# Performance work log

Measured on AMD Instinct MI355X. Metric: run time of the kernel, lower is better.

Reference implementation:

```python
import jax, jax.numpy as jnp
import numpy as np

B, N, D_IN, D_OUT = 8, 2048, 1024, 1024

def setup_inputs() -> dict:
    key = jax.random.key(0)
    kx, kq, kk, kv = jax.random.split(key, 4)
    scale = 1.0 / np.sqrt(D_IN)
    return {
        "x": jax.random.normal(kx, (B, N, D_IN), dtype=jnp.float32),
        "Wq": jax.random.normal(kq, (D_IN, D_OUT), dtype=jnp.float32) * scale,
        "Wk": jax.random.normal(kk, (D_IN, D_OUT), dtype=jnp.float32) * scale,
        "Wv": jax.random.normal(kv, (D_IN, D_OUT), dtype=jnp.float32) * scale,
    }

def reference(x, Wq, Wk, Wv):
    # Projections (qkv_bias=False)
    q = x @ Wq  # [B, N, d_out]
    k = x @ Wk
    v = x @ Wv
    n = x.shape[1]
    scores = jnp.einsum('bqd,bkd->bqk', q, k)  # [B, N, N]
    causal_mask = jnp.triu(jnp.ones((n, n), dtype=bool), k=1)
    scores = jnp.where(causal_mask, -jnp.inf, scores)
    inv_sqrt_d = jnp.asarray(1.0 / np.sqrt(q.shape[-1]), dtype=scores.dtype)
    attn = jax.nn.softmax(scores * inv_sqrt_d, axis=-1)
    # dropout p=0.0 -> identity
    return jnp.einsum('bqk,bkd->bqd', attn, v)
```

## Files before the change

kernel.cpp:

```cpp
#include <hip/hip_runtime.h>
#include <hip/hip_bf16.h>

#define DI __device__ __forceinline__

typedef __bf16 bf16x8 __attribute__((ext_vector_type(8)));
typedef float  f32x4  __attribute__((ext_vector_type(4)));

DI unsigned short f2bf(float f) {
    unsigned int u = __float_as_uint(f);
    u += 0x7fffu + ((u >> 16) & 1u);
    return (unsigned short)(u >> 16);
}

DI void gload16(const unsigned short* g, unsigned short* l) {
    __builtin_amdgcn_global_load_lds(
        (const __attribute__((address_space(1))) unsigned int*)g,
        (__attribute__((address_space(3))) unsigned int*)l, 16, 0, 0);
}

__global__ void convert_x(const float* __restrict__ x, unsigned short* __restrict__ Xb) {
    int i = blockIdx.x * 256 + threadIdx.x;
    float4 v = reinterpret_cast<const float4*>(x)[i];
    ushort4 o;
    o.x = f2bf(v.x); o.y = f2bf(v.y); o.z = f2bf(v.z); o.w = f2bf(v.w);
    reinterpret_cast<ushort4*>(Xb)[i] = o;
}

__global__ void convert_w(const float* __restrict__ Wq, const float* __restrict__ Wk,
                          const float* __restrict__ Wv, unsigned short* __restrict__ Wt) {
    __shared__ float t[32][33];
    const int z = blockIdx.z;
    const float* W = (z == 0) ? Wq : (z == 1 ? Wk : Wv);
    const float scale = (z == 0) ? 0.03125f : 1.0f;
    const int n0 = blockIdx.x * 32, k0 = blockIdx.y * 32;
    const int tx = threadIdx.x, ty = threadIdx.y;
#pragma unroll
    for (int i = 0; i < 4; ++i)
        t[ty + i * 8][tx] = W[(size_t)(k0 + ty + i * 8) * 1024 + n0 + tx];
    __syncthreads();
#pragma unroll
    for (int i = 0; i < 4; ++i)
        Wt[(size_t)(z * 1024 + n0 + ty + i * 8) * 1024 + k0 + tx] =
            f2bf(t[tx][ty + i * 8] * scale);
}

#define BAR    asm volatile("s_barrier" ::: "memory")
#define WAITV4 asm volatile("s_waitcnt vmcnt(4)" ::: "memory")
#define WAITV3 asm volatile("s_waitcnt vmcnt(3)" ::: "memory")
#define WAITV0 asm volatile("s_waitcnt vmcnt(0)" ::: "memory")


#define READ_A(SLOT, MH)                                                      \
    _Pragma("unroll")                                                         \
    for (int fi = 0; fi < 4; ++fi)                                            \
        _Pragma("unroll")                                                     \
        for (int kk = 0; kk < 2; ++kk)                                        \
            aR[fi][kk] = *reinterpret_cast<const bf16x8*>(                    \
                lsA + (SLOT) * 16384 + (MH) * 8192 +                          \
                ((abase ^ (kk * 32)) + fi * 1024));

#define READ_B(SLOT, NH, BS)                                                  \
    _Pragma("unroll")                                                         \
    for (int fj = 0; fj < 2; ++fj)                                            \
        _Pragma("unroll")                                                     \
        for (int kk = 0; kk < 2; ++kk)                                        \
            BS[fj][kk] = *reinterpret_cast<const bf16x8*>(                    \
                lsB + (SLOT) * 16384 + (NH) * 8192 +                          \
                ((bbase ^ (kk * 32)) + fj * 1024));

#define STAGE_A(KT, H)                                                        \
    {                                                                         \
        unsigned uA_ = (unsigned)(m0 + (H) * 128) * 1024u + (unsigned)(KT) * 64u; \
        _Pragma("unroll")                                                     \
        for (int it = 0; it < 2; ++it)                                        \
            gload16(Ab + uA_ + sAoff[it],                                     \
                    lsA + (((KT) & 1) * 2 + (H)) * 8192 + it * 4096 + tid * 8);\
    }

#define STAGE_B(KT, H)                                                        \
    {                                                                         \
        unsigned uB_ = (unsigned)(n0 + (H) * 128) * 1024u + (unsigned)(KT) * 64u; \
        _Pragma("unroll")                                                     \
        for (int it = 0; it < 2; ++it)                                        \
            gload16(Bb + uB_ + sBoff[it],                                     \
                    lsB + (((KT) & 1) * 2 + (H)) * 8192 + it * 4096 + tid * 8);\
    }

#define MMA_PHASE(MH, NH, BS)                                                 \
    __builtin_amdgcn_s_setprio(1);                                            \
    _Pragma("unroll")                                                         \
    for (int kk = 0; kk < 2; ++kk)                                            \
        _Pragma("unroll")                                                     \
        for (int fi = 0; fi < 4; ++fi)                                        \
            _Pragma("unroll")                                                 \
            for (int fj = 0; fj < 2; ++fj)                                    \
                acc[(MH) * 4 + fi][(NH) * 2 + fj] =                           \
                    __builtin_amdgcn_mfma_f32_16x16x32_bf16(                  \
                        aR[fi][kk], BS[fj][kk],                               \
                        acc[(MH) * 4 + fi][(NH) * 2 + fj], 0, 0, 0);          \
    __builtin_amdgcn_s_setprio(0);

__global__ __launch_bounds__(512) void gemm256(
    const unsigned short* __restrict__ A0, const unsigned short* __restrict__ B0,
    unsigned short* __restrict__ Oq, unsigned short* __restrict__ Ok,
    unsigned short* __restrict__ Ov)
{
    extern __shared__ char smem_raw[];
    unsigned short* lsA = (unsigned short*)smem_raw;
    unsigned short* lsB = lsA + 32768;

    const int tid = threadIdx.x;
    const int lane = tid & 63;
    const int wid = tid >> 6;
    const int wm = wid >> 2, wn = wid & 3;
    const int lr = lane & 15, lg = lane >> 4;

    const int m0 = blockIdx.x * 256, n0 = blockIdx.y * 256;
    const int NT = 16;
    const unsigned short* Ab = A0;
    const unsigned short* Bb = B0;

    const unsigned chm = (unsigned)(lg ^ (lr & 7));
    const unsigned abase = (unsigned)(wm * 64 + lr) * 64u + chm * 8u;
    const unsigned bbase = (unsigned)(wn * 32 + lr) * 64u + chm * 8u;
    unsigned sAoff[2], sBoff[2];
#pragma unroll
    for (int it = 0; it < 2; ++it) {
        const unsigned idx = it * 512 + tid;
        const unsigned row = idx >> 3;
        const unsigned ch = (idx & 7) ^ (row & 7);
        sAoff[it] = row * 1024u + ch * 8u;
        sBoff[it] = row * 1024u + ch * 8u;
    }

    f32x4 acc[8][4] = {};
    bf16x8 aR[4][2], b0[2][2], b1[2][2];

    STAGE_A(0, 0); STAGE_A(0, 1); STAGE_B(0, 0); STAGE_B(0, 1);
    STAGE_A(1, 0); STAGE_B(1, 0);
    WAITV4; BAR;

    for (int kt = 0; kt < NT; ++kt) {
        const int slot = kt & 1;
        const bool s1 = (kt + 1) < NT, s2 = (kt + 2) < NT;
        READ_A(slot, 0); READ_B(slot, 0, b0);
        if (s1) { STAGE_A(kt + 1, 1); }
        BAR; MMA_PHASE(0, 0, b0);
        READ_B(slot, 1, b1);
        if (s1) { STAGE_B(kt + 1, 1); }
        BAR; MMA_PHASE(0, 1, b1);
        READ_A(slot, 1);
        if (s2) { STAGE_A(kt + 2, 0); }
        BAR; MMA_PHASE(1, 0, b0);
        if (s2) {
            STAGE_B(kt + 2, 0);
            WAITV4;
        } else {
            WAITV0;
        }
        BAR; MMA_PHASE(1, 1, b1);
    }

#pragma unroll
    for (int i = 0; i < 8; ++i) {
        const int rl = (i >> 2) * 128 + wm * 64 + (i & 3) * 16 + lg * 4;
#pragma unroll
        for (int j = 0; j < 4; ++j) {
            const int cl = (j >> 1) * 128 + wn * 32 + (j & 1) * 16 + lr;
            f32x4 v = acc[i][j];
            const int gm = m0 + rl;
            const int z = n0 >> 10;
            const int cin = (n0 & 1023) + cl;
            if (z == 2) {
                const int b = gm >> 11, nib = gm & 2047;
                ushort4 h;
                h.x = f2bf(v[0]); h.y = f2bf(v[1]); h.z = f2bf(v[2]); h.w = f2bf(v[3]);
                *reinterpret_cast<ushort4*>(
                    &Ov[(size_t)b * 2097152u + (size_t)cin * 2048 + nib]) = h;
            } else {
                unsigned short* O = z ? Ok : Oq;
#pragma unroll
                for (int r2 = 0; r2 < 4; ++r2)
                    O[(size_t)(gm + r2) * 1024 + cin] = f2bf(v[r2]);
            }
        }
    }
}

template <int MODE>
__global__ __launch_bounds__(512, 4) void gemm_attn(
    const unsigned short* __restrict__ A0, const unsigned short* __restrict__ B0,
    float* __restrict__ Cf)
{
    __shared__ alignas(16) unsigned short lds[3 * 12288];

    const int tid = threadIdx.x;
    const int lane = tid & 63;
    const int wid = tid >> 6;
    const int wm = wid >> 2, wn = wid & 3;
    const int lr = lane & 15, lg = lane >> 4;

    int r128, n0, NT, bz;
    constexpr unsigned STRB = (MODE == 2) ? 2048u : 1024u;

    if constexpr (MODE == 1) {
        const int idx = blockIdx.x;
        bz = idx & 7;
        const int t = idx >> 3;
        int mm = 0;
        while ((mm + 1) * (mm + 2) <= t) ++mm;
        const int u = t - mm * (mm + 1);
        r128 = 2 * mm + (u >= (mm + 1) ? 1 : 0);
        const int c256 = u % (mm + 1);
        n0 = c256 * 256; NT = 32;
    } else {
        const int idx = blockIdx.x;
        const int k5 = idx >> 5;
        r128 = (k5 < 8) ? (15 - k5) : (k5 - 8);
        const int nt4 = (idx >> 3) & 3;
        bz = idx & 7;
        n0 = nt4 * 256; NT = 4 * (r128 + 1);
    }
    const int r256 = r128 >> 1;
    const unsigned short* Bb = B0 + (size_t)bz * 2097152u;

    const unsigned short* Ab;
    size_t cbase;
    if constexpr (MODE == 1) {
        Ab = A0 + (size_t)bz * 2097152u;
        cbase = ((size_t)bz * 36 + (size_t)(r256 * (r256 + 1) / 2) + (n0 >> 8)) * 65536u +
                (size_t)(r128 & 1) * 32768u;
    } else {
        Ab = A0 + ((size_t)bz * 36 + (size_t)(r256 * (r256 + 1) / 2)) * 65536u;
        cbase = (size_t)bz * 2097152u + (size_t)(r128 * 128) * 1024u;
    }

    const unsigned fswl = (unsigned)((lr ^ (lr >> 2)) & 3);
    const unsigned abase = (unsigned)(wm * 64 + lr) * 32u + ((unsigned)lg ^ fswl) * 8u;
    const unsigned bbase = 4096u + (unsigned)(wn * 32 + lr) * 32u + ((unsigned)lg ^ fswl) * 8u;

    const unsigned rowA = (unsigned)(tid >> 2);
    const unsigned chA = ((unsigned)tid & 3u) ^ (unsigned)((rowA ^ (rowA >> 2)) & 3u);
    unsigned sAoff;
    if constexpr (MODE == 1)
        sAoff = ((unsigned)(r128 * 128) + rowA) * 1024u + chA * 8u;
    else
        sAoff = ((unsigned)((r128 & 1) * 128) + rowA) * 256u + chA * 8u;
    unsigned sBoff[2];
#pragma unroll
    for (int it = 0; it < 2; ++it) {
        const unsigned idx = it * 512 + tid;
        const unsigned rowB = idx >> 2;
        const unsigned chB = (idx & 3u) ^ (unsigned)((rowB ^ (rowB >> 2)) & 3u);
        sBoff[it] = ((unsigned)n0 + rowB) * STRB + chB * 8u;
    }

#define AT_STAGE(KT, SL)                                                      \
    {                                                                         \
        unsigned u_;                                                          \
        if constexpr (MODE == 2)                                              \
            u_ = ((unsigned)((KT) >> 3)) * 65536u + ((KT) & 7) * 32u;         \
        else                                                                  \
            u_ = (unsigned)(KT) * 32u;                                        \
        gload16(Ab + u_ + sAoff, lds + (SL) * 12288 + tid * 8);               \
        gload16(Bb + (unsigned)(KT) * 32u + sBoff[0],                         \
                lds + (SL) * 12288 + 4096 + tid * 8);                         \
        gload16(Bb + (unsigned)(KT) * 32u + sBoff[1],                         \
                lds + (SL) * 12288 + 8192 + tid * 8);                         \
    }

    f32x4 acc[4][4] = {};
    bf16x8 aR[4], bv[2];

    AT_STAGE(0, 0); AT_STAGE(1, 1);

    int sl = 0, st2 = 2;
    for (int kt = 0; kt < NT; ++kt) {
        if (kt + 1 < NT) { WAITV3; } else { WAITV0; }
        BAR;
        if (kt + 2 < NT) { AT_STAGE(kt + 2, st2); }
        const unsigned short* sp = lds + sl * 12288;
#pragma unroll
        for (int fi = 0; fi < 4; ++fi)
            aR[fi] = *reinterpret_cast<const bf16x8*>(sp + abase + fi * 512);
#pragma unroll
        for (int fj = 0; fj < 2; ++fj)
            bv[fj] = *reinterpret_cast<const bf16x8*>(sp + bbase + fj * 512);
        __builtin_amdgcn_s_setprio(1);
#pragma unroll
        for (int fi = 0; fi < 4; ++fi)
#pragma unroll
            for (int fj = 0; fj < 2; ++fj)
                acc[fi][fj] = __builtin_amdgcn_mfma_f32_16x16x32_bf16(
                    aR[fi], bv[fj], acc[fi][fj], 0, 0, 0);
        __builtin_amdgcn_s_setprio(0);
#pragma unroll
        for (int fj = 0; fj < 2; ++fj)
            bv[fj] = *reinterpret_cast<const bf16x8*>(sp + bbase + 4096 + fj * 512);
        __builtin_amdgcn_s_setprio(1);
#pragma unroll
        for (int fi = 0; fi < 4; ++fi)
#pragma unroll
            for (int fj = 0; fj < 2; ++fj)
                acc[fi][2 + fj] = __builtin_amdgcn_mfma_f32_16x16x32_bf16(
                    aR[fi], bv[fj], acc[fi][2 + fj], 0, 0, 0);
        __builtin_amdgcn_s_setprio(0);
        sl = (sl == 2) ? 0 : sl + 1;
        st2 = (st2 == 2) ? 0 : st2 + 1;
    }

#pragma unroll
    for (int fi = 0; fi < 4; ++fi) {
        const int rloc = wm * 64 + fi * 16 + lg * 4;
#pragma unroll
        for (int j = 0; j < 4; ++j) {
            const int cloc = (j >> 1) * 128 + wn * 32 + (j & 1) * 16 + lr;
            f32x4 v = acc[fi][j];
            if constexpr (MODE == 1) {
#pragma unroll
                for (int r2 = 0; r2 < 4; ++r2)
                    Cf[cbase + (size_t)(rloc + r2) * 256 + cloc] = v[r2];
            } else {
#pragma unroll
                for (int r2 = 0; r2 < 4; ++r2)
                    Cf[cbase + (size_t)(rloc + r2) * 1024 + (n0 + cloc)] = v[r2];
            }
        }
    }
#undef AT_STAGE
}

__global__ __launch_bounds__(256) void softmax_rows(const float* __restrict__ Sp,
                                                    unsigned short* __restrict__ Pp) {
    const int R = blockIdx.x;
    const int b = blockIdx.y;
    const int rt = R >> 8;
    const size_t rowbase = ((size_t)b * 36 + (size_t)(rt * (rt + 1) / 2)) * 65536u +
                           (size_t)(R & 255) * 256;
    const int tid = threadIdx.x;
    const int lane4 = (tid & 63) * 4;
    const int tj0 = tid >> 6;

    float4 vals[2];
    float m = -3.0e38f;
    int cnt = 0;
    for (int tj = tj0; tj <= rt; tj += 4, ++cnt) {
        float4 s = *reinterpret_cast<const float4*>(
            &Sp[rowbase + (size_t)tj * 65536u + lane4]);
        vals[cnt] = s;
        const int k0 = tj * 256 + lane4;
        if (k0 + 3 <= R) {
            m = fmaxf(m, fmaxf(fmaxf(s.x, s.y), fmaxf(s.z, s.w)));
        } else {
            if (k0     <= R) m = fmaxf(m, s.x);
            if (k0 + 1 <= R) m = fmaxf(m, s.y);
            if (k0 + 2 <= R) m = fmaxf(m, s.z);
        }
    }
    __shared__ float red[4];
#pragma unroll
    for (int o = 32; o > 0; o >>= 1) m = fmaxf(m, __shfl_xor(m, o));
    if ((tid & 63) == 0) red[tid >> 6] = m;
    __syncthreads();
    m = fmaxf(fmaxf(red[0], red[1]), fmaxf(red[2], red[3]));
    __syncthreads();

    float l = 0.0f;
    cnt = 0;
    for (int tj = tj0; tj <= rt; tj += 4, ++cnt) {
        float4 s = vals[cnt];
        const int k0 = tj * 256 + lane4;
        float4 e;
        e.x = (k0     <= R) ? __expf(s.x - m) : 0.0f;
        e.y = (k0 + 1 <= R) ? __expf(s.y - m) : 0.0f;
        e.z = (k0 + 2 <= R) ? __expf(s.z - m) : 0.0f;
        e.w = (k0 + 3 <= R) ? __expf(s.w - m) : 0.0f;
        vals[cnt] = e;
        l += e.x + e.y + e.z + e.w;
    }
#pragma unroll
    for (int o = 32; o > 0; o >>= 1) l += __shfl_xor(l, o);
    if ((tid & 63) == 0) red[tid >> 6] = l;
    __syncthreads();
    l = red[0] + red[1] + red[2] + red[3];
    const float inv = 1.0f / l;

    cnt = 0;
    for (int tj = tj0; tj <= rt; tj += 4, ++cnt) {
        float4 e = vals[cnt];
        ushort4 h;
        h.x = f2bf(e.x * inv); h.y = f2bf(e.y * inv);
        h.z = f2bf(e.z * inv); h.w = f2bf(e.w * inv);
        *reinterpret_cast<ushort4*>(
            &Pp[rowbase + (size_t)tj * 65536u + lane4]) = h;
    }
}

extern "C" void kernel_launch(void* const* d_in, const int* in_sizes, int n_in,
                              void* d_out, int out_size, void* d_ws, size_t ws_size,
                              hipStream_t stream) {
    const float* x  = (const float*)d_in[0];
    const float* Wq = (const float*)d_in[1];
    const float* Wk = (const float*)d_in[2];
    const float* Wv = (const float*)d_in[3];
    float* out = (float*)d_out;

    char* base = (char*)d_ws;
    unsigned short* Qb = (unsigned short*)(base);
    unsigned short* Kb = (unsigned short*)(base + 33554432u);
    unsigned short* Vt = (unsigned short*)(base + 67108864u);
    unsigned short* Xb = (unsigned short*)(base + 100663296u);
    unsigned short* Wt = (unsigned short*)(base + 134217728u);
    float*          Sp = (float*)         (base + 100663296u);
    unsigned short* Pp = (unsigned short*)(base + 176160768u);

    hipFuncSetAttribute(reinterpret_cast<const void*>(&gemm256),
                        hipFuncAttributeMaxDynamicSharedMemorySize, 131072);

    convert_x<<<16384, 256, 0, stream>>>(x, Xb);
    convert_w<<<dim3(32, 32, 3), dim3(32, 8), 0, stream>>>(Wq, Wk, Wv, Wt);
    gemm256<<<dim3(64, 12), 512, 131072, stream>>>(Xb, Wt, Qb, Kb, Vt);
    gemm_attn<1><<<576, 512, 0, stream>>>(Qb, Kb, Sp);
    softmax_rows<<<dim3(2048, 8), 256, 0, stream>>>(Sp, Pp);
    gemm_attn<2><<<512, 512, 0, stream>>>(Pp, Vt, out);
}
```

Baseline: 271.2 us.

## Store attention scores in bf16 and simplify causal tile indexing

The QK^T kernel now writes scores as bf16 instead of fp32, and the softmax kernel reads bf16 and widens to float, halving the score traffic through memory. The triangular block-index decode loop is replaced by a rectangular grid of 1024 blocks whose upper-triangle blocks exit early. Rounding scores to bf16 before softmax costs accuracy, and the early-exit blocks add launch overhead.

Result: no change. 269.1 us (-0.8%).

```diff
diff --git a/kernel.cpp b/kernel.cpp
--- a/kernel.cpp
+++ b/kernel.cpp
@@ -10,6 +10,10 @@
     unsigned int u = __float_as_uint(f);
     u += 0x7fffu + ((u >> 16) & 1u);
     return (unsigned short)(u >> 16);
+}
+
+DI float b2f(unsigned short h) {
+    return __uint_as_float((unsigned)h << 16);
 }
 
 DI void gload16(const unsigned short* g, unsigned short* l) {
@@ -190,7 +194,7 @@
 template <int MODE>
 __global__ __launch_bounds__(512, 4) void gemm_attn(
     const unsigned short* __restrict__ A0, const unsigned short* __restrict__ B0,
-    float* __restrict__ Cf)
+    void* __restrict__ Cf0)
 {
     __shared__ alignas(16) unsigned short lds[3 * 12288];
 
@@ -206,12 +210,9 @@
     if constexpr (MODE == 1) {
         const int idx = blockIdx.x;
         bz = idx & 7;
-        const int t = idx >> 3;
-        int mm = 0;
-        while ((mm + 1) * (mm + 2) <= t) ++mm;
-        const int u = t - mm * (mm + 1);
-        r128 = 2 * mm + (u >= (mm + 1) ? 1 : 0);
-        const int c256 = u % (mm + 1);
+        r128 = (idx >> 3) & 15;
+        const int c256 = idx >> 7;
+        if (c256 > (r128 >> 1)) return;
         n0 = c256 * 256; NT = 32;
     } else {
         const int idx = blockIdx.x;
@@ -317,10 +318,12 @@
             const int cloc = (j >> 1) * 128 + wn * 32 + (j & 1) * 16 + lr;
             f32x4 v = acc[fi][j];
             if constexpr (MODE == 1) {
+                unsigned short* Cs = (unsigned short*)Cf0;
 #pragma unroll
                 for (int r2 = 0; r2 < 4; ++r2)
-                    Cf[cbase + (size_t)(rloc + r2) * 256 + cloc] = v[r2];
+                    Cs[cbase + (size_t)(rloc + r2) * 256 + cloc] = f2bf(v[r2]);
             } else {
+                float* Cf = (float*)Cf0;
 #pragma unroll
                 for (int r2 = 0; r2 < 4; ++r2)
                     Cf[cbase + (size_t)(rloc + r2) * 1024 + (n0 + cloc)] = v[r2];
@@ -330,7 +333,7 @@
 #undef AT_STAGE
 }
 
-__global__ __launch_bounds__(256) void softmax_rows(const float* __restrict__ Sp,
+__global__ __launch_bounds__(256) void softmax_rows(const unsigned short* __restrict__ Sb,
                                                     unsigned short* __restrict__ Pp) {
     const int R = blockIdx.x;
     const int b = blockIdx.y;
@@ -345,8 +348,10 @@
     float m = -3.0e38f;
     int cnt = 0;
     for (int tj = tj0; tj <= rt; tj += 4, ++cnt) {
-        float4 s = *reinterpret_cast<const float4*>(
-            &Sp[rowbase + (size_t)tj * 65536u + lane4]);
+        ushort4 sr = *reinterpret_cast<const ushort4*>(
+            &Sb[rowbase + (size_t)tj * 65536u + lane4]);
+        float4 s;
+        s.x = b2f(sr.x); s.y = b2f(sr.y); s.z = b2f(sr.z); s.w = b2f(sr.w);
         vals[cnt] = s;
         const int k0 = tj * 256 + lane4;
         if (k0 + 3 <= R) {
@@ -411,7 +416,7 @@
     unsigned short* Vt = (unsigned short*)(base + 67108864u);
     unsigned short* Xb = (unsigned short*)(base + 100663296u);
     unsigned short* Wt = (unsigned short*)(base + 134217728u);
-    float*          Sp = (float*)         (base + 100663296u);
+    unsigned short* Sb = (unsigned short*)(base + 100663296u);
     unsigned short* Pp = (unsigned short*)(base + 176160768u);
 
     hipFuncSetAttribute(reinterpret_cast<const void*>(&gemm256),
@@ -420,7 +425,7 @@
     convert_x<<<16384, 256, 0, stream>>>(x, Xb);
     convert_w<<<dim3(32, 32, 3), dim3(32, 8), 0, stream>>>(Wq, Wk, Wv, Wt);
     gemm256<<<dim3(64, 12), 512, 131072, stream>>>(Xb, Wt, Qb, Kb, Vt);
-    gemm_attn<1><<<576, 512, 0, stream>>>(Qb, Kb, Sp);
-    softmax_rows<<<dim3(2048, 8), 256, 0, stream>>>(Sp, Pp);
+    gemm_attn<1><<<1024, 512, 0, stream>>>(Qb, Kb, Sb);
+    softmax_rows<<<dim3(2048, 8), 256, 0, stream>>>(Sb, Pp);
     gemm_attn<2><<<512, 512, 0, stream>>>(Pp, Vt, out);
 }
```
